# Performance work log

Measured on AMD Instinct MI355X. Metric: run time of the kernel, lower is better.

The kernel has to match this reference:

```python
import jax, jax.numpy as jnp
import numpy as np

B, E, D = 4096, 64, 1024

def setup_inputs() -> dict:
    key = jax.random.key(0)
    k1, k2 = jax.random.split(key)
    z = jax.random.normal(k1, (B, D), dtype=jnp.float32)
    expert_keys = jax.random.normal(k2, (E, D), dtype=jnp.float32)
    log_sigma = jnp.zeros((D,), dtype=jnp.float32)
    return {"z": z, "expert_keys": expert_keys, "log_sigma": log_sigma}

def reference(z, expert_keys, log_sigma):
    # diag(sigma_inv) @ diff followed by (. * diff).sum(-1) is exactly an
    # elementwise-scaled squared distance: sum_d exp(-log_sigma_d) * diff_d^2
    sigma_inv = jnp.exp(-log_sigma)                              # [D]
    diff = z[:, None, :] - expert_keys[None, :, :]               # [B, E, D]
    mahalanobis_dist = jnp.einsum('bed,d,bed->be', diff, sigma_inv, diff)  # [B, E]
    similarity = 1.0 / (1.0 + mahalanobis_dist)                  # [B, E]
    weights = jax.nn.softmax(similarity, axis=-1)                # [B, E]
    weighted_expert = weights @ expert_keys                      # [B, D]
    return (similarity, weighted_expert)
```

## Files before the change

### kernel.cpp

```cpp
#include <hip/hip_runtime.h>
#include <hip/hip_bf16.h>

#define B_N 4096
#define E_N 64
#define D_N 1024
#define ROWS 16

typedef __bf16 bf16x8 __attribute__((ext_vector_type(8)));
typedef __bf16 bf16x4 __attribute__((ext_vector_type(4)));
typedef float f32x4 __attribute__((ext_vector_type(4)));


__global__ __launch_bounds__(256) void prep_kernel(
    const float* __restrict__ keys, const float* __restrict__ lsig,
    float* __restrict__ sinv, float* __restrict__ ak,
    __bf16* __restrict__ sk, __bf16* __restrict__ kT)
{
  __shared__ float red[4];
  __shared__ __bf16 tl[64][72];
  const int bid = blockIdx.x;
  const int t = threadIdx.x;

  if (bid < 64) {
    const int e = bid;
    const float4 k4 = *(const float4*)(keys + e * D_N + 4 * t);
    const float4 l4 = *(const float4*)(lsig + 4 * t);
    float4 s4;
    s4.x = expf(-l4.x); s4.y = expf(-l4.y); s4.z = expf(-l4.z); s4.w = expf(-l4.w);
    if (e == 0) *(float4*)(sinv + 4 * t) = s4;
    const float4 sk4 = make_float4(s4.x * k4.x, s4.y * k4.y, s4.z * k4.z, s4.w * k4.w);
    bf16x4 skb;
    skb[0] = (__bf16)sk4.x; skb[1] = (__bf16)sk4.y; skb[2] = (__bf16)sk4.z; skb[3] = (__bf16)sk4.w;
    *(bf16x4*)(sk + e * D_N + 4 * t) = skb;
    float p = sk4.x * k4.x + sk4.y * k4.y + sk4.z * k4.z + sk4.w * k4.w;
    #pragma unroll
    for (int off = 32; off > 0; off >>= 1) p += __shfl_down(p, off);
    if ((t & 63) == 0) red[t >> 6] = p;
    __syncthreads();
    if (t == 0) ak[e] = red[0] + red[1] + red[2] + red[3];
  } else {
    const int d0 = (bid - 64) * 64;
    #pragma unroll
    for (int p = 0; p < 4; ++p) {
      const int e  = p * 16 + (t >> 4);
      const int dd = (t & 15) * 4;
      const float4 k4 = *(const float4*)(keys + (size_t)e * D_N + d0 + dd);
      tl[dd + 0][e] = (__bf16)k4.x; tl[dd + 1][e] = (__bf16)k4.y;
      tl[dd + 2][e] = (__bf16)k4.z; tl[dd + 3][e] = (__bf16)k4.w;
    }
    __syncthreads();
    #pragma unroll
    for (int p = 0; p < 2; ++p) {
      const int dd = p * 32 + (t >> 3);
      const int l8 = t & 7;
      const bf16x8 v = *(const bf16x8*)&tl[dd][l8 * 8];
      *(bf16x8*)(kT + (size_t)(d0 + dd) * E_N + l8 * 8) = v;
    }
  }
}

__global__ __launch_bounds__(512, 2) void main_kernel(
    const float* __restrict__ z, const float* __restrict__ sinv,
    const float* __restrict__ ak, const __bf16* __restrict__ sk,
    const __bf16* __restrict__ kT,
    float* __restrict__ out_sim, float* __restrict__ out_we)
{
  constexpr int ZS = D_N + 8;
  __shared__ __bf16 zlds[ROWS * ZS];
  __shared__ float azs[ROWS];
  __shared__ float pacc[2][4][16][20];
  __shared__ __bf16 wlds[ROWS][72];

  const int t  = threadIdx.x;
  const int b0 = blockIdx.x * ROWS;

  const int wave = t >> 6;
  const int lane = t & 63;
  const int ln = lane & 15;
  const int q  = lane >> 4;
  const int et = wave & 3;
  const int kh = wave >> 2;

  f32x4 ak4 = {0.f, 0.f, 0.f, 0.f};
  if (t < 256) ak4 = *(const f32x4*)(ak + (t & 15) * 4);

  const int sr = t >> 5;
  const int sc = t & 31;
  const float* zrow = z + (size_t)(b0 + sr) * D_N;
  float az = 0.f;
  #pragma unroll
  for (int l = 0; l < 8; ++l) {
    const int c = sc * 4 + l * 128;
    const float4 z4 = *(const float4*)(zrow + c);
    const float4 s4 = *(const float4*)(sinv + c);
    az += s4.x * z4.x * z4.x + s4.y * z4.y * z4.y + s4.z * z4.z * z4.z + s4.w * z4.w * z4.w;
    bf16x4 zb;
    zb[0] = (__bf16)z4.x; zb[1] = (__bf16)z4.y; zb[2] = (__bf16)z4.z; zb[3] = (__bf16)z4.w;
    *(bf16x4*)(&zlds[sr * ZS + c]) = zb;
  }
  az += __shfl_xor(az, 1);  az += __shfl_xor(az, 2);
  az += __shfl_xor(az, 4);  az += __shfl_xor(az, 8);
  az += __shfl_xor(az, 16);
  if (sc == 0) azs[sr] = az;

  const __bf16* bp = sk + (size_t)(et * 16 + ln) * D_N + kh * 512 + q * 8;
  const bf16x8 bpf0 = *(const bf16x8*)(bp);
  const bf16x8 bpf1 = *(const bf16x8*)(bp + 32);
  const bf16x8 bpf2 = *(const bf16x8*)(bp + 64);
  const bf16x8 bpf3 = *(const bf16x8*)(bp + 96);

  __syncthreads();

  const __bf16* ap = &zlds[ln * ZS + kh * 512 + q * 8];
  f32x4 acc = {0.f, 0.f, 0.f, 0.f};
  {
    const bf16x8 a0 = *(const bf16x8*)(ap);
    acc = __builtin_amdgcn_mfma_f32_16x16x32_bf16(a0, bpf0, acc, 0, 0, 0);
    const bf16x8 a1 = *(const bf16x8*)(ap + 32);
    acc = __builtin_amdgcn_mfma_f32_16x16x32_bf16(a1, bpf1, acc, 0, 0, 0);
    const bf16x8 a2 = *(const bf16x8*)(ap + 64);
    acc = __builtin_amdgcn_mfma_f32_16x16x32_bf16(a2, bpf2, acc, 0, 0, 0);
    const bf16x8 a3 = *(const bf16x8*)(ap + 96);
    acc = __builtin_amdgcn_mfma_f32_16x16x32_bf16(a3, bpf3, acc, 0, 0, 0);
  }
  #pragma unroll
  for (int ks = 4; ks < 16; ++ks) {
    const bf16x8 bfr = *(const bf16x8*)(bp + ks * 32);
    const bf16x8 afr = *(const bf16x8*)(ap + ks * 32);
    acc = __builtin_amdgcn_mfma_f32_16x16x32_bf16(afr, bfr, acc, 0, 0, 0);
  }

  #pragma unroll
  for (int i = 0; i < 4; ++i) pacc[kh][et][q * 4 + i][ln] = acc[i];

  bf16x8 pb0a, pb0b, pb1a, pb1b, pb2a, pb2b, pb3a, pb3b;
  {
    const __bf16* kp;
    kp = kT + (size_t)((wave +  0) * 16 + ln) * E_N + q * 8;
    pb0a = *(const bf16x8*)(kp); pb0b = *(const bf16x8*)(kp + 32);
    kp = kT + (size_t)((wave +  8) * 16 + ln) * E_N + q * 8;
    pb1a = *(const bf16x8*)(kp); pb1b = *(const bf16x8*)(kp + 32);
    kp = kT + (size_t)((wave + 16) * 16 + ln) * E_N + q * 8;
    pb2a = *(const bf16x8*)(kp); pb2b = *(const bf16x8*)(kp + 32);
    kp = kT + (size_t)((wave + 24) * 16 + ln) * E_N + q * 8;
    pb3a = *(const bf16x8*)(kp); pb3b = *(const bf16x8*)(kp + 32);
  }

  __syncthreads();

  if (t < 256) {
    const int row = t >> 4, seg = t & 15;
    const f32x4 p0 = *(const f32x4*)&pacc[0][seg >> 2][row][(seg & 3) * 4];
    const f32x4 p1 = *(const f32x4*)&pacc[1][seg >> 2][row][(seg & 3) * 4];
    const float azr = azs[row];
    f32x4 s;
    #pragma unroll
    for (int j = 0; j < 4; ++j) {
      const float dist = azr + ak4[j] - 2.0f * (p0[j] + p1[j]);
      s[j] = 1.0f / (1.0f + dist);
    }
    *(f32x4*)(out_sim + (size_t)(b0 + row) * E_N + seg * 4) = s;
    float mx = fmaxf(fmaxf(s[0], s[1]), fmaxf(s[2], s[3]));
    mx = fmaxf(mx, __shfl_xor(mx, 1));
    mx = fmaxf(mx, __shfl_xor(mx, 2));
    mx = fmaxf(mx, __shfl_xor(mx, 4));
    mx = fmaxf(mx, __shfl_xor(mx, 8));
    float v[4];
    float sum = 0.f;
    #pragma unroll
    for (int j = 0; j < 4; ++j) { v[j] = __expf(s[j] - mx); sum += v[j]; }
    sum += __shfl_xor(sum, 1);
    sum += __shfl_xor(sum, 2);
    sum += __shfl_xor(sum, 4);
    sum += __shfl_xor(sum, 8);
    const float inv = 1.0f / sum;
    bf16x4 wq;
    #pragma unroll
    for (int j = 0; j < 4; ++j) wq[j] = (__bf16)(v[j] * inv);
    *(bf16x4*)&wlds[row][seg * 4] = wq;
  }
  __syncthreads();

  const bf16x8 a0 = *(const bf16x8*)&wlds[ln][q * 8];
  const bf16x8 a1 = *(const bf16x8*)&wlds[ln][32 + q * 8];
  #pragma unroll
  for (int i = 0; i < 8; ++i) {
    const int dt = wave + 8 * i;
    const int d0 = dt * 16;
    bf16x8 b0f, b1f;
    if      (i == 0) { b0f = pb0a; b1f = pb0b; }
    else if (i == 1) { b0f = pb1a; b1f = pb1b; }
    else if (i == 2) { b0f = pb2a; b1f = pb2b; }
    else if (i == 3) { b0f = pb3a; b1f = pb3b; }
    else {
      const __bf16* kp = kT + (size_t)(d0 + ln) * E_N + q * 8;
      b0f = *(const bf16x8*)(kp);
      b1f = *(const bf16x8*)(kp + 32);
    }
    f32x4 o = {0.f, 0.f, 0.f, 0.f};
    o = __builtin_amdgcn_mfma_f32_16x16x32_bf16(a0, b0f, o, 0, 0, 0);
    o = __builtin_amdgcn_mfma_f32_16x16x32_bf16(a1, b1f, o, 0, 0, 0);
    #pragma unroll
    for (int j = 0; j < 4; ++j)
      out_we[(size_t)(b0 + q * 4 + j) * D_N + d0 + ln] = o[j];
  }
}

extern "C" void kernel_launch(void* const* d_in, const int* in_sizes, int n_in,
                              void* d_out, int out_size, void* d_ws, size_t ws_size,
                              hipStream_t stream)
{
  const float* z    = (const float*)d_in[0];
  const float* keys = (const float*)d_in[1];
  const float* ls   = (const float*)d_in[2];
  float* out_sim = (float*)d_out;
  float* out_we  = out_sim + (size_t)B_N * E_N;
  char* ws = (char*)d_ws;
  float*  sinv = (float*)(ws);
  float*  ak   = (float*)(ws + 4096);
  __bf16* sk   = (__bf16*)(ws + 4352);
  __bf16* kT   = (__bf16*)(ws + 135424);
  prep_kernel<<<80, 256, 0, stream>>>(keys, ls, sinv, ak, sk, kT);
  main_kernel<<<B_N / ROWS, 512, 0, stream>>>(z, sinv, ak, sk, kT, out_sim, out_we);
}
```

Measured before the change: 84.45 us.

## Double block size to 1024 threads with 4-way K split in main kernel

Launches main_kernel with 1024 threads (16 waves) instead of 512. The distance GEMM's K dimension is split four ways instead of two, with partial sums reduced through a larger LDS buffer, and each wave now computes 4 instead of 8 D-tiles of the weighted-expert product. The early prefetch of key fragments into registers before the barriers is dropped. The intent is more waves per block to hide latency and shorter per-wave serial chains, at the cost of losing the prefetch overlap and changing occupancy (the launch bound no longer requests 2 blocks per CU).

New measurement: 81.55 us. -3.4%, faster.

```diff
diff --git a/kernel.cpp b/kernel.cpp
--- a/kernel.cpp
+++ b/kernel.cpp
@@ -59,7 +59,7 @@
   }
 }
 
-__global__ __launch_bounds__(512, 2) void main_kernel(
+__global__ __launch_bounds__(1024) void main_kernel(
     const float* __restrict__ z, const float* __restrict__ sinv,
     const float* __restrict__ ak, const __bf16* __restrict__ sk,
     const __bf16* __restrict__ kT,
@@ -68,7 +68,7 @@
   constexpr int ZS = D_N + 8;
   __shared__ __bf16 zlds[ROWS * ZS];
   __shared__ float azs[ROWS];
-  __shared__ float pacc[2][4][16][20];
+  __shared__ float pacc[4][4][16][20];
   __shared__ __bf16 wlds[ROWS][72];
 
   const int t  = threadIdx.x;
@@ -79,18 +79,18 @@
   const int ln = lane & 15;
   const int q  = lane >> 4;
   const int et = wave & 3;
-  const int kh = wave >> 2;
+  const int kq = wave >> 2;
 
   f32x4 ak4 = {0.f, 0.f, 0.f, 0.f};
   if (t < 256) ak4 = *(const f32x4*)(ak + (t & 15) * 4);
 
-  const int sr = t >> 5;
-  const int sc = t & 31;
+  const int sr = wave;
+  const int sc = lane;
   const float* zrow = z + (size_t)(b0 + sr) * D_N;
   float az = 0.f;
   #pragma unroll
-  for (int l = 0; l < 8; ++l) {
-    const int c = sc * 4 + l * 128;
+  for (int l = 0; l < 4; ++l) {
+    const int c = sc * 4 + l * 256;
     const float4 z4 = *(const float4*)(zrow + c);
     const float4 s4 = *(const float4*)(sinv + c);
     az += s4.x * z4.x * z4.x + s4.y * z4.y * z4.y + s4.z * z4.z * z4.z + s4.w * z4.w * z4.w;
@@ -100,63 +100,39 @@
   }
   az += __shfl_xor(az, 1);  az += __shfl_xor(az, 2);
   az += __shfl_xor(az, 4);  az += __shfl_xor(az, 8);
-  az += __shfl_xor(az, 16);
+  az += __shfl_xor(az, 16); az += __shfl_xor(az, 32);
   if (sc == 0) azs[sr] = az;
-
-  const __bf16* bp = sk + (size_t)(et * 16 + ln) * D_N + kh * 512 + q * 8;
-  const bf16x8 bpf0 = *(const bf16x8*)(bp);
-  const bf16x8 bpf1 = *(const bf16x8*)(bp + 32);
-  const bf16x8 bpf2 = *(const bf16x8*)(bp + 64);
-  const bf16x8 bpf3 = *(const bf16x8*)(bp + 96);
 
   __syncthreads();
 
-  const __bf16* ap = &zlds[ln * ZS + kh * 512 + q * 8];
+  const __bf16* bp = sk + (size_t)(et * 16 + ln) * D_N + kq * 256 + q * 8;
+  const __bf16* ap = &zlds[ln * ZS + kq * 256 + q * 8];
   f32x4 acc = {0.f, 0.f, 0.f, 0.f};
-  {
-    const bf16x8 a0 = *(const bf16x8*)(ap);
-    acc = __builtin_amdgcn_mfma_f32_16x16x32_bf16(a0, bpf0, acc, 0, 0, 0);
-    const bf16x8 a1 = *(const bf16x8*)(ap + 32);
-    acc = __builtin_amdgcn_mfma_f32_16x16x32_bf16(a1, bpf1, acc, 0, 0, 0);
-    const bf16x8 a2 = *(const bf16x8*)(ap + 64);
-    acc = __builtin_amdgcn_mfma_f32_16x16x32_bf16(a2, bpf2, acc, 0, 0, 0);
-    const bf16x8 a3 = *(const bf16x8*)(ap + 96);
-    acc = __builtin_amdgcn_mfma_f32_16x16x32_bf16(a3, bpf3, acc, 0, 0, 0);
-  }
   #pragma unroll
-  for (int ks = 4; ks < 16; ++ks) {
+  for (int ks = 0; ks < 8; ++ks) {
     const bf16x8 bfr = *(const bf16x8*)(bp + ks * 32);
     const bf16x8 afr = *(const bf16x8*)(ap + ks * 32);
     acc = __builtin_amdgcn_mfma_f32_16x16x32_bf16(afr, bfr, acc, 0, 0, 0);
   }
-
   #pragma unroll
-  for (int i = 0; i < 4; ++i) pacc[kh][et][q * 4 + i][ln] = acc[i];
-
-  bf16x8 pb0a, pb0b, pb1a, pb1b, pb2a, pb2b, pb3a, pb3b;
-  {
-    const __bf16* kp;
-    kp = kT + (size_t)((wave +  0) * 16 + ln) * E_N + q * 8;
-    pb0a = *(const bf16x8*)(kp); pb0b = *(const bf16x8*)(kp + 32);
-    kp = kT + (size_t)((wave +  8) * 16 + ln) * E_N + q * 8;
-    pb1a = *(const bf16x8*)(kp); pb1b = *(const bf16x8*)(kp + 32);
-    kp = kT + (size_t)((wave + 16) * 16 + ln) * E_N + q * 8;
-    pb2a = *(const bf16x8*)(kp); pb2b = *(const bf16x8*)(kp + 32);
-    kp = kT + (size_t)((wave + 24) * 16 + ln) * E_N + q * 8;
-    pb3a = *(const bf16x8*)(kp); pb3b = *(const bf16x8*)(kp + 32);
-  }
+  for (int i = 0; i < 4; ++i) pacc[kq][et][q * 4 + i][ln] = acc[i];
 
   __syncthreads();
 
   if (t < 256) {
     const int row = t >> 4, seg = t & 15;
-    const f32x4 p0 = *(const f32x4*)&pacc[0][seg >> 2][row][(seg & 3) * 4];
-    const f32x4 p1 = *(const f32x4*)&pacc[1][seg >> 2][row][(seg & 3) * 4];
+    const int pe = seg >> 2, pc = (seg & 3) * 4;
+    f32x4 p = *(const f32x4*)&pacc[0][pe][row][pc];
+    #pragma unroll
+    for (int k = 1; k < 4; ++k) {
+      const f32x4 pk = *(const f32x4*)&pacc[k][pe][row][pc];
+      p[0] += pk[0]; p[1] += pk[1]; p[2] += pk[2]; p[3] += pk[3];
+    }
     const float azr = azs[row];
     f32x4 s;
     #pragma unroll
     for (int j = 0; j < 4; ++j) {
-      const float dist = azr + ak4[j] - 2.0f * (p0[j] + p1[j]);
+      const float dist = azr + ak4[j] - 2.0f * p[j];
       s[j] = 1.0f / (1.0f + dist);
     }
     *(f32x4*)(out_sim + (size_t)(b0 + row) * E_N + seg * 4) = s;
@@ -184,19 +160,12 @@
   const bf16x8 a0 = *(const bf16x8*)&wlds[ln][q * 8];
   const bf16x8 a1 = *(const bf16x8*)&wlds[ln][32 + q * 8];
   #pragma unroll
-  for (int i = 0; i < 8; ++i) {
-    const int dt = wave + 8 * i;
+  for (int i = 0; i < 4; ++i) {
+    const int dt = wave + 16 * i;
     const int d0 = dt * 16;
-    bf16x8 b0f, b1f;
-    if      (i == 0) { b0f = pb0a; b1f = pb0b; }
-    else if (i == 1) { b0f = pb1a; b1f = pb1b; }
-    else if (i == 2) { b0f = pb2a; b1f = pb2b; }
-    else if (i == 3) { b0f = pb3a; b1f = pb3b; }
-    else {
-      const __bf16* kp = kT + (size_t)(d0 + ln) * E_N + q * 8;
-      b0f = *(const bf16x8*)(kp);
-      b1f = *(const bf16x8*)(kp + 32);
-    }
+    const __bf16* kp = kT + (size_t)(d0 + ln) * E_N + q * 8;
+    const bf16x8 b0f = *(const bf16x8*)(kp);
+    const bf16x8 b1f = *(const bf16x8*)(kp + 32);
     f32x4 o = {0.f, 0.f, 0.f, 0.f};
     o = __builtin_amdgcn_mfma_f32_16x16x32_bf16(a0, b0f, o, 0, 0, 0);
     o = __builtin_amdgcn_mfma_f32_16x16x32_bf16(a1, b1f, o, 0, 0, 0);
@@ -221,5 +190,5 @@
   __bf16* sk   = (__bf16*)(ws + 4352);
   __bf16* kT   = (__bf16*)(ws + 135424);
   prep_kernel<<<80, 256, 0, stream>>>(keys, ls, sinv, ak, sk, kT);
-  main_kernel<<<B_N / ROWS, 512, 0, stream>>>(z, sinv, ak, sk, kT, out_sim, out_we);
+  main_kernel<<<B_N / ROWS, 1024, 0, stream>>>(z, sinv, ak, sk, kT, out_sim, out_we);
 }
```
